# Kernel optimization log

Measured on AMD Instinct MI355X. Metric: run time of the kernel, lower is better.

Reference implementation:

```python
import jax, jax.numpy as jnp
import numpy as np

B, C, H, W = 1, 512, 64, 64
HEADS, DH = 8, 64
DI = HEADS * DH          # 512 = heads * dim_head
SW = 8                   # sliding window size
CB = 16                  # compress block size
SB = 2                   # selection block size
NSEL = 2                 # num selected blocks
N = H * W                # 4096 tokens
NCB = N // CB            # 256 compress blocks
NFB = N // SB            # 2048 fine (selection) blocks
NEG = jnp.finfo(jnp.float32).min


def setup_inputs() -> dict:
    key = jax.random.key(0)
    ks = jax.random.split(key, 24)
    rn = lambda k, shape, s=0.03: jax.random.normal(k, shape, jnp.float32) * s
    return dict(
        x=jax.random.normal(ks[0], (B, C, H, W), jnp.float32),
        w_in=rn(ks[1], (C, C)), b_in=jnp.zeros((C,), jnp.float32),
        g_norm=jnp.ones((C,), jnp.float32),
        wq=rn(ks[2], (DI, C)), wk=rn(ks[3], (DI, C)), wv=rn(ks[4], (DI, C)),
        k_pos=rn(ks[5], (HEADS, CB, DH), 0.02), v_pos=rn(ks[6], (HEADS, CB, DH), 0.02),
        mem_k=rn(ks[7], (HEADS, 1, DH), 0.02), mem_v=rn(ks[8], (HEADS, 1, DH), 0.02),
        kc_w1=rn(ks[9], (CB * DH, CB * DH)), kc_b1=jnp.zeros((CB * DH,), jnp.float32),
        kc_w2=rn(ks[10], (DH, CB * DH)), kc_b2=jnp.zeros((DH,), jnp.float32),
        vc_w1=rn(ks[11], (CB * DH, CB * DH)), vc_b1=jnp.zeros((CB * DH,), jnp.float32),
        vc_w2=rn(ks[12], (DH, CB * DH)), vc_b2=jnp.zeros((DH,), jnp.float32),
        w_strat=rn(ks[13], (3 * HEADS, C)), b_strat=jnp.zeros((3 * HEADS,), jnp.float32),
        w_comb=rn(ks[14], (C, DI)),
        w_out=rn(ks[15], (C, C)), b_out=jnp.zeros((C,), jnp.float32),
    )


def _rope(x):
    # rotary-embedding-torch default: theta=10000, interleaved pairs
    d = x.shape[-1]
    inv = 1.0 / (10000.0 ** (jnp.arange(0, d, 2, dtype=jnp.float32) / d))
    ang = jnp.arange(x.shape[-2], dtype=jnp.float32)[:, None] * inv  # (n, d/2)
    cos = jnp.repeat(jnp.cos(ang), 2, axis=-1)
    sin = jnp.repeat(jnp.sin(ang), 2, axis=-1)
    xp = x.reshape(x.shape[:-1] + (d // 2, 2))
    xr = jnp.stack((-xp[..., 1], xp[..., 0]), axis=-1).reshape(x.shape)
    return x * cos + xr * sin


def reference(x, w_in, b_in, g_norm, wq, wk, wv, k_pos, v_pos, mem_k, mem_v,
              kc_w1, kc_b1, kc_w2, kc_b2, vc_w1, vc_b1, vc_w2, vc_b2,
              w_strat, b_strat, w_comb, w_out, b_out):
    scale = DH ** -0.5
    # proj_in (1x1 conv) then flatten to sequence (b, n, c); residual uses this
    xs = jnp.einsum('bchw,oc->bohw', x, w_in) + b_in[None, :, None, None]
    seq = xs.reshape(B, C, N).transpose(0, 2, 1)
    # RMSNorm
    h = seq * jax.lax.rsqrt(jnp.mean(seq * seq, -1, keepdims=True) + 1e-6) * g_norm
    # qkv -> (b, heads, n, d)
    q = (h @ wq.T).reshape(B, N, HEADS, DH).transpose(0, 2, 1, 3)
    k = (h @ wk.T).reshape(B, N, HEADS, DH).transpose(0, 2, 1, 3)
    v = (h @ wv.T).reshape(B, N, HEADS, DH).transpose(0, 2, 1, 3)

    # ---- 1. compressed attention (block compression MLP + mem kv) ----
    kin = (k + jnp.tile(k_pos, (1, NCB, 1))[None]).reshape(B, HEADS, NCB, CB * DH)
    vin = (v + jnp.tile(v_pos, (1, NCB, 1))[None]).reshape(B, HEADS, NCB, CB * DH)
    ck = jax.nn.relu(kin @ kc_w1.T + kc_b1) @ kc_w2.T + kc_b2   # (b,h,NCB,d)
    cv = jax.nn.relu(vin @ vc_w1.T + vc_b1) @ vc_w2.T + vc_b2
    ck = jnp.concatenate([jnp.broadcast_to(mem_k[None], (B, HEADS, 1, DH)), ck], axis=2)
    cv = jnp.concatenate([jnp.broadcast_to(mem_v[None], (B, HEADS, 1, DH)), cv], axis=2)
    ck_seq = jnp.concatenate([jnp.array([-1]), (jnp.arange(NCB) + 1) * CB - 1])
    cmask = ck_seq[None, :] < jnp.arange(N)[:, None]             # (N, NCB+1), True=attend
    csim = jnp.einsum('bhid,bhjd->bhij', q, ck) * scale
    csim = jnp.where(cmask[None, None], csim, NEG)
    compressed_out = jnp.einsum('bhij,bhjd->bhid', jax.nn.softmax(csim, axis=-1), cv)

    # rotary positions for fine + sliding branches
    rq, rk = _rope(q), _rope(k)

    # ---- 2. fine selection attention ----
    # importance at fine-block granularity; since SB divides CB, each fine block
    # maps to exactly one compress block (equivalent to repeat->mask->mean in torch)
    imp = csim[..., 1:]                                          # drop mem kv logits
    fb_of = jnp.arange(NFB) // (CB // SB)
    imp_fine = imp[..., fb_of]                                   # (b,h,N,NFB)
    blk_causal = jnp.arange(NFB)[None, :] < (jnp.arange(N) // SB)[:, None]
    imp_fine = jnp.where(blk_causal[None, None], imp_fine, -jnp.inf)
    logits = jnp.concatenate([jnp.full((B, HEADS, N, 1), -1e3, jnp.float32), imp_fine], axis=-1)
    probs = jax.nn.softmax(logits, axis=-1)[..., 1:]             # (b,h,N,NFB)
    sel_val, sel_idx = jax.lax.top_k(probs, NSEL)                # (b,h,N,NSEL)
    diag_idx = jnp.broadcast_to((jnp.arange(N) // SB)[None, None, :, None], (B, HEADS, N, 1))
    sel_idx = jnp.concatenate([sel_idx, diag_idx], axis=-1)      # append own (diagonal) block
    fmask_sel = jnp.repeat((sel_val > 1e-10)[..., None], SB, axis=-1)   # (b,h,N,NSEL,SB)
    diag_mask = jnp.arange(SB)[None, :] <= (jnp.arange(N) % SB)[:, None]  # within-block causal
    diag_mask = jnp.broadcast_to(diag_mask[None, None, :, None, :], (B, HEADS, N, 1, SB))
    fmask = jnp.concatenate([fmask_sel, diag_mask], axis=-2).reshape(B, HEADS, N, (NSEL + 1) * SB)
    fk_blk = rk.reshape(B, HEADS, NFB, SB, DH)
    fv_blk = v.reshape(B, HEADS, NFB, SB, DH)
    idx = sel_idx.reshape(B, HEADS, N * (NSEL + 1))[..., None, None]
    fk = jnp.take_along_axis(fk_blk, idx, axis=2).reshape(B, HEADS, N, (NSEL + 1) * SB, DH)
    fv = jnp.take_along_axis(fv_blk, idx, axis=2).reshape(B, HEADS, N, (NSEL + 1) * SB, DH)
    fsim = jnp.einsum('bhid,bhijd->bhij', rq, fk) * scale
    fsim = jnp.where(fmask, fsim, NEG)
    fine_out = jnp.einsum('bhij,bhijd->bhid', jax.nn.softmax(fsim, axis=-1), fv)

    # ---- 3. sliding window attention (causal, exact window: 0 <= i-j <= SW) ----
    kp = jnp.pad(rk, ((0, 0), (0, 0), (SW, 0), (0, 0)))
    vp = jnp.pad(v, ((0, 0), (0, 0), (SW, 0), (0, 0)))
    widx = jnp.arange(N)[:, None] + jnp.arange(SW + 1)[None, :]  # indices into padded seq
    kw = kp[:, :, widx]                                          # (b,h,N,SW+1,d)
    vw = vp[:, :, widx]
    wvalid = (jnp.arange(N)[:, None] - SW + jnp.arange(SW + 1)[None, :]) >= 0
    ssim = jnp.einsum('bhid,bhijd->bhij', rq, kw) * scale
    ssim = jnp.where(wvalid[None, None], ssim, NEG)
    slide_out = jnp.einsum('bhij,bhijd->bhid', jax.nn.softmax(ssim, axis=-1), vw)

    # ---- combine the three strategies with learned sigmoid gates ----
    gates = jax.nn.sigmoid(h @ w_strat.T + b_strat).reshape(B, N, HEADS, 3).transpose(0, 2, 1, 3)
    out = gates[..., 0:1] * compressed_out + gates[..., 1:2] * fine_out + gates[..., 2:3] * slide_out
    out = out.transpose(0, 2, 1, 3).reshape(B, N, DI) @ w_comb.T  # merge heads + combine
    out2d = out.transpose(0, 2, 1).reshape(B, C, H, W)
    return jnp.einsum('bchw,oc->bohw', out2d, w_out) + b_out[None, :, None, None] + xs
```

## Files before the change

kernel.cpp:

```cpp
#include <hip/hip_runtime.h>
#include <hip/hip_bf16.h>
#include <math.h>

typedef __attribute__((ext_vector_type(8))) short s8v;
typedef __attribute__((ext_vector_type(8))) _Float16 h8v;
typedef __attribute__((ext_vector_type(4))) float f4v;
typedef __hip_bfloat16 bf16;

#define NEGF (-3.40282346638528859812e+38f)
#define QSMEM 10240
#define BSMEM 10240

enum { EPI_F32 = 0, EPI_BIAS, EPI_BRELU_BF16, EPI_BF16, EPI_FINAL };

__device__ __forceinline__ float wred_sum(float v) {
#pragma unroll
  for (int m = 1; m < 64; m <<= 1) v += __shfl_xor(v, m, 64);
  return v;
}

template <int EPI>
__device__ __forceinline__ void bgemm_body(char* smem, int bx, int by, int bz,
    const bf16* __restrict__ A, const bf16* __restrict__ B, void* __restrict__ C,
    int K, int ldC, long sA, long sB, long sC,
    const float* __restrict__ bias, const void* __restrict__ aux) {
  short (*Bhs)[2560] = (short(*)[2560])smem;
  const short* ah = (const short*)A + (long)bz * sA;
  const short* bh = (const short*)B + (long)bz * sB;
  int tid = threadIdx.x;
  int wv_ = tid >> 6, lane = tid & 63;
  int lrow = tid >> 2, lcol = (tid & 3) << 3;
  int lidx = lrow * 40 + lcol;
  long bbase = (long)(by * 64 + lrow) * K + lcol;
  int frow = lane & 15, fk = (lane >> 4) << 3;
  long aga = (long)(bx * 64 + wv_ * 16 + frow) * K + fk;
  f4v acc[4] = {};
  { *(s8v*)&Bhs[0][lidx] = *(const s8v*)&bh[bbase]; }
  __syncthreads();
  int nit = K >> 5, buf = 0;
  s8v rA, rB, sE, sO;
  sE = *(const s8v*)&ah[aga];
  if (nit > 1) {
    rA = *(const s8v*)&bh[bbase + 32];
    sO = *(const s8v*)&ah[aga + 32];
  }
#define B_MFMA(sreg)                                                   \
  {                                                                    \
    _Pragma("unroll") for (int nt = 0; nt < 4; nt++) {                 \
      s8v bfh = *(const s8v*)&Bhs[buf][(nt * 16 + frow) * 40 + fk];    \
      acc[nt] = __builtin_amdgcn_mfma_f32_16x16x32_bf16(sreg, bfh, acc[nt], 0, 0, 0); \
    }                                                                  \
  }
  for (int it = 0; it < nit; it += 2) {
    if (it + 2 < nit) rB = *(const s8v*)&bh[bbase + ((long)(it + 2) << 5)];
    B_MFMA(sE)
    if (it + 2 < nit) sE = *(const s8v*)&ah[aga + ((long)(it + 2) << 5)];
    if (it + 1 < nit) {
      *(s8v*)&Bhs[buf ^ 1][lidx] = rA;
      __syncthreads();
      buf ^= 1;
      if (it + 3 < nit) rA = *(const s8v*)&bh[bbase + ((long)(it + 3) << 5)];
      B_MFMA(sO)
      if (it + 3 < nit) sO = *(const s8v*)&ah[aga + ((long)(it + 3) << 5)];
      if (it + 2 < nit) {
        *(s8v*)&Bhs[buf ^ 1][lidx] = rB;
        __syncthreads();
        buf ^= 1;
      }
    }
  }
#undef B_MFMA
  int rb = bx * 64 + wv_ * 16 + ((lane >> 4) << 2);
#pragma unroll
  for (int nt = 0; nt < 4; nt++) {
    int gn = by * 64 + nt * 16 + (lane & 15);
#pragma unroll
    for (int rg = 0; rg < 4; rg++) {
      int gm = rb + rg;
      float v = acc[nt][rg];
      long ci = (long)bz * sC + (long)gm * ldC + gn;
      if (EPI == EPI_F32) ((float*)C)[ci] = v;
      else if (EPI == EPI_BIAS) ((float*)C)[ci] = v + bias[gn];
      else if (EPI == EPI_BRELU_BF16) ((bf16*)C)[ci] = __float2bfloat16(fmaxf(v + bias[gn], 0.f));
      else if (EPI == EPI_BF16) ((bf16*)C)[ci] = __float2bfloat16(v);
      else if (EPI == EPI_FINAL)
        ((float*)C)[ci] = v + bias[gm] + ((const float*)aux)[(long)gn * 512 + gm];
    }
  }
}


#define HX_DECL                                                     \
  short* L = (short*)smem;                                          \
  const int MS = 64 * 40;                                           \
  int tid = threadIdx.x;                                            \
  int wv = tid >> 6, lane = tid & 63;                               \
  int lrow = tid >> 2, lcol = (tid & 3) << 3;                       \
  int frow = lane & 15, fk = (lane >> 4) << 3;                      \
  int soff = lrow * 40 + lcol;                                      \
  f4v acc0[4] = {}, accx[4] = {};

#define HX_STAGE0                                                   \
  {                                                                 \
    *(h8v*)&L[soff] = *(const h8v*)&Bh[bbase];                      \
    *(h8v*)&L[MS + soff] = *(const h8v*)&Bl[bbase];                 \
  }                                                                 \
  __syncthreads();

#define HX_MFMA(sah, sal)                                           \
  {                                                                 \
    _Pragma("unroll") for (int nt = 0; nt < 4; nt++) {              \
      int bo = (nt * 16 + frow) * 40 + fk;                          \
      h8v bh_ = *(const h8v*)&L[bo];                                \
      h8v bl_ = *(const h8v*)&L[MS + bo];                           \
      acc0[nt] = __builtin_amdgcn_mfma_f32_16x16x32_f16(sah, bh_, acc0[nt], 0, 0, 0); \
      accx[nt] = __builtin_amdgcn_mfma_f32_16x16x32_f16(sah, bl_, accx[nt], 0, 0, 0); \
      accx[nt] = __builtin_amdgcn_mfma_f32_16x16x32_f16(sal, bh_, accx[nt], 0, 0, 0); \
    }                                                               \
  }

#define HX_LOOP(NIT)                                                \
  h8v rAh, rAl, rBh, rBl, sEh, sEl, sOh, sOl;                       \
  sEh = *(const h8v*)&Ah[aga];                                      \
  sEl = *(const h8v*)&Al[aga];                                      \
  if ((NIT) > 1) {                                                  \
    rAh = *(const h8v*)&Bh[bbase + 32];                             \
    rAl = *(const h8v*)&Bl[bbase + 32];                             \
    sOh = *(const h8v*)&Ah[aga + 32];                               \
    sOl = *(const h8v*)&Al[aga + 32];                               \
  }                                                                 \
  for (int it = 0; it < (NIT); it += 2) {                           \
    if (it + 2 < (NIT)) {                                           \
      long ko = (long)(it + 2) << 5;                                \
      rBh = *(const h8v*)&Bh[bbase + ko];                           \
      rBl = *(const h8v*)&Bl[bbase + ko];                           \
    }                                                               \
    HX_MFMA(sEh, sEl)                                               \
    if (it + 2 < (NIT)) {                                           \
      long ko = (long)(it + 2) << 5;                                \
      sEh = *(const h8v*)&Ah[aga + ko];                             \
      sEl = *(const h8v*)&Al[aga + ko];                             \
    }                                                               \
    if (it + 1 < (NIT)) {                                           \
      __syncthreads();                                              \
      *(h8v*)&L[soff] = rAh;                                        \
      *(h8v*)&L[MS + soff] = rAl;                                   \
      __syncthreads();                                              \
      if (it + 3 < (NIT)) {                                         \
        long ko = (long)(it + 3) << 5;                              \
        rAh = *(const h8v*)&Bh[bbase + ko];                         \
        rAl = *(const h8v*)&Bl[bbase + ko];                         \
      }                                                             \
      HX_MFMA(sOh, sOl)                                             \
      if (it + 3 < (NIT)) {                                         \
        long ko = (long)(it + 3) << 5;                              \
        sOh = *(const h8v*)&Ah[aga + ko];                           \
        sOl = *(const h8v*)&Al[aga + ko];                           \
      }                                                             \
      if (it + 2 < (NIT)) {                                         \
        __syncthreads();                                            \
        *(h8v*)&L[soff] = rBh;                                      \
        *(h8v*)&L[MS + soff] = rBl;                                 \
        __syncthreads();                                            \
      }                                                             \
    }                                                               \
  }

#define HX_COMBINE(nt, rg) (acc0[nt][rg] + accx[nt][rg] * (1.f / 4096.f))

__device__ __forceinline__ void qk_f16_body(char* smem, int bx, int by,
    const _Float16* __restrict__ Ah, const _Float16* __restrict__ Al,
    const _Float16* __restrict__ Bh, const _Float16* __restrict__ Bl,
    _Float16* __restrict__ qhh, _Float16* __restrict__ qhl,
    _Float16* __restrict__ kinh, _Float16* __restrict__ kinl,
    float* __restrict__ rq, float* __restrict__ rk, const float* __restrict__ kpos,
    const float2* __restrict__ ropet) {
  HX_DECL
  long aga = (long)(bx * 64 + wv * 16 + frow) * 512 + fk;
  long bbase = (long)(by * 64 + lrow) * 512 + lcol;
  HX_STAGE0
  HX_LOOP(16)
  bool isq = by < 8;
  int h = by & 7;
  int rb = wv * 16 + ((lane >> 4) << 2);
#pragma unroll
  for (int nt = 0; nt < 4; nt++) {
    int dloc = nt * 16 + frow;
    int d2 = dloc >> 1;
#pragma unroll
    for (int rg = 0; rg < 4; rg++) {
      int n = bx * 64 + rb + rg;
      float vf = HX_COMBINE(nt, rg);
      float2 cs = ropet[(long)n * 32 + d2];
      float sv = cs.x, cv = cs.y;
      float vp = __shfl_xor(vf, 1, 64);
      float rr = (dloc & 1) ? (vf * cv + vp * sv) : (vf * cv - vp * sv);
      long oi = ((long)h * 4096 + n) * 64 + dloc;
      if (isq) {
        _Float16 hi = (_Float16)vf;
        qhh[oi] = hi;
        qhl[oi] = (_Float16)((vf - (float)hi) * 4096.f);
        rq[oi] = rr;
      } else {
        rk[oi] = rr;
        float kv = vf + kpos[(h * 16 + (n & 15)) * 64 + dloc];
        _Float16 khi = (_Float16)kv;
        long ki = (((long)h * 256 + (n >> 4)) * 16 + (n & 15)) * 64 + dloc;
        kinh[ki] = khi;
        kinl[ki] = (_Float16)((kv - (float)khi) * 4096.f);
      }
    }
  }
}

__device__ __forceinline__ void hx_conv_body(char* smem, int bx, int by,
    const _Float16* __restrict__ Ah, const _Float16* __restrict__ Al,
    const _Float16* __restrict__ Bh, const _Float16* __restrict__ Bl,
    float* __restrict__ C, const float* __restrict__ bias) {
  HX_DECL
  long aga = (long)(bx * 64 + wv * 16 + frow) * 512 + fk;
  long bbase = (long)(by * 64 + lrow) * 512 + lcol;
  HX_STAGE0
  HX_LOOP(16)
  int rb = bx * 64 + wv * 16 + ((lane >> 4) << 2);
#pragma unroll
  for (int nt = 0; nt < 4; nt++) {
    int gn = by * 64 + nt * 16 + frow;
#pragma unroll
    for (int rg = 0; rg < 4; rg++) {
      int gm = rb + rg;
      C[(long)gm * 512 + gn] = HX_COMBINE(nt, rg) + bias[gn];
    }
  }
}

__device__ __forceinline__ void hx_mlp1_body(char* smem, int bx, int by,
    const _Float16* __restrict__ Ah, const _Float16* __restrict__ Al,
    const _Float16* __restrict__ Bh, const _Float16* __restrict__ Bl,
    _Float16* __restrict__ Ch, _Float16* __restrict__ Cl, const float* __restrict__ bias) {
  HX_DECL
  long aga = (long)(bx * 64 + wv * 16 + frow) * 1024 + fk;
  long bbase = (long)(by * 64 + lrow) * 1024 + lcol;
  HX_STAGE0
  HX_LOOP(32)
  int rb = bx * 64 + wv * 16 + ((lane >> 4) << 2);
#pragma unroll
  for (int nt = 0; nt < 4; nt++) {
    int gn = by * 64 + nt * 16 + frow;
#pragma unroll
    for (int rg = 0; rg < 4; rg++) {
      int gm = rb + rg;
      float v = fmaxf(HX_COMBINE(nt, rg) + bias[gn], 0.f);
      _Float16 hi = (_Float16)v;
      long ci = (long)gm * 1024 + gn;
      Ch[ci] = hi;
      Cl[ci] = (_Float16)((v - (float)hi) * 4096.f);
    }
  }
}

__device__ __forceinline__ void hx_ksplit_body(char* smem, int bx, int by,
    const _Float16* __restrict__ Ah, const _Float16* __restrict__ Al,
    const _Float16* __restrict__ Bh, const _Float16* __restrict__ Bl,
    float* __restrict__ P) {
  HX_DECL
  long kbeg = (long)by << 7;
  long aga = (long)(bx * 64 + wv * 16 + frow) * 1024 + kbeg + fk;
  long bbase = (long)lrow * 1024 + kbeg + lcol;
  HX_STAGE0
  HX_LOOP(4)
  float* p = P + (long)by * 131072;
  int rb = bx * 64 + wv * 16 + ((lane >> 4) << 2);
#pragma unroll
  for (int nt = 0; nt < 4; nt++) {
    int gn = nt * 16 + frow;
#pragma unroll
    for (int rg = 0; rg < 4; rg++) {
      int gm = rb + rg;
      p[(long)gm * 64 + gn] = HX_COMBINE(nt, rg);
    }
  }
}

__device__ __forceinline__ void hx_csim_body(char* smem, int bx, int by, int bz,
    const _Float16* __restrict__ Ah, const _Float16* __restrict__ Al,
    const _Float16* __restrict__ Bh, const _Float16* __restrict__ Bl,
    float* __restrict__ C) {
  HX_DECL
  long aga = ((long)bz * 4096 + bx * 64 + wv * 16 + frow) * 64 + fk;
  long bbase = ((long)bz * 320 + by * 64 + lrow) * 64 + lcol;
  HX_STAGE0
  HX_LOOP(2)
  int rb = bx * 64 + wv * 16 + ((lane >> 4) << 2);
#pragma unroll
  for (int nt = 0; nt < 4; nt++) {
    int gn = by * 64 + nt * 16 + frow;
#pragma unroll
    for (int rg = 0; rg < 4; rg++) {
      int gm = rb + rg;
      C[((long)bz * 4096 + gm) * 320 + gn] = HX_COMBINE(nt, rg) * 0.125f;
    }
  }
}

__device__ __forceinline__ void prep_elem(long i,
    const float* __restrict__ wq, const float* __restrict__ wk, const float* __restrict__ wv,
    const float* __restrict__ wst, const float* __restrict__ bst,
    const float* __restrict__ kc_w1, const float* __restrict__ kc_w2,
    const float* __restrict__ vc_w1, const float* __restrict__ vc_w2, const float* __restrict__ w_comb,
    const float* __restrict__ w_out, _Float16* __restrict__ wqkh, _Float16* __restrict__ wqkl,
    bf16* __restrict__ wvs, float* __restrict__ bias2,
    _Float16* __restrict__ kw1h, _Float16* __restrict__ kw1l,
    _Float16* __restrict__ kw2h, _Float16* __restrict__ kw2l, bf16* __restrict__ vw1b,
    bf16* __restrict__ vw2b, bf16* __restrict__ wcombb, bf16* __restrict__ woutb) {
  if (i < 524288) {
    int r = (int)(i >> 9), c = (int)(i & 511);
    float w = (r < 512) ? wq[i] : wk[(r - 512) * 512 + c];
    _Float16 hi = (_Float16)w;
    wqkh[i] = hi;
    wqkl[i] = (_Float16)((w - (float)hi) * 4096.f);
    return;
  }
  i -= 524288;
  if (i < 294912) {
    int r = (int)(i >> 9), c = (int)(i & 511);
    float v = 0.f;
    if (r < 512) v = wv[i];
    else if (r < 536) v = wst[(r - 512) * 512 + c];
    wvs[i] = __float2bfloat16(v);
    if (i < 576) bias2[i] = (i >= 512 && i < 536) ? bst[i - 512] : 0.f;
    return;
  }
  i -= 294912;
  if (i < 1048576) {
    float w = kc_w1[i];
    _Float16 hi = (_Float16)w;
    kw1h[i] = hi;
    kw1l[i] = (_Float16)((w - (float)hi) * 4096.f);
    return;
  }
  i -= 1048576;
  if (i < 65536) {
    float w = kc_w2[i];
    _Float16 hi = (_Float16)w;
    kw2h[i] = hi;
    kw2l[i] = (_Float16)((w - (float)hi) * 4096.f);
    return;
  }
  i -= 65536;
  if (i < 1048576) { vw1b[i] = __float2bfloat16(vc_w1[i]); return; }
  i -= 1048576;
  if (i < 65536) { vw2b[i] = __float2bfloat16(vc_w2[i]); return; }
  i -= 65536;
  if (i < 262144) { wcombb[i] = __float2bfloat16(w_comb[i]); return; }
  i -= 262144;
  if (i < 262144) woutb[i] = __float2bfloat16(w_out[i]);
}
#define PREP_TOTAL 3571712l

template <int EPI>
__global__ __launch_bounds__(256) void gemm_bt(
    const bf16* __restrict__ A, const bf16* __restrict__ B, void* __restrict__ C,
    int K, int ldC, long sA, long sB, long sC,
    const float* __restrict__ bias, const void* __restrict__ aux) {
  __shared__ char smem[BSMEM];
  bgemm_body<EPI>(smem, blockIdx.x, blockIdx.y, blockIdx.z, A, B, C, K, ldC, sA, sB, sC, bias, aux);
}

__global__ __launch_bounds__(256) void k_conv_prep(
    const _Float16* __restrict__ xth, const _Float16* __restrict__ xtl,
    const _Float16* __restrict__ winh, const _Float16* __restrict__ winl,
    float* __restrict__ xsf, const float* __restrict__ b_in,
    const float* __restrict__ wq, const float* __restrict__ wk, const float* __restrict__ wv,
    const float* __restrict__ wst, const float* __restrict__ bst,
    const float* __restrict__ kc_w1, const float* __restrict__ kc_w2,
    const float* __restrict__ vc_w1, const float* __restrict__ vc_w2, const float* __restrict__ w_comb,
    const float* __restrict__ w_out, _Float16* __restrict__ wqkh, _Float16* __restrict__ wqkl,
    bf16* __restrict__ wvs, float* __restrict__ bias2,
    _Float16* __restrict__ kw1h, _Float16* __restrict__ kw1l,
    _Float16* __restrict__ kw2h, _Float16* __restrict__ kw2l, bf16* __restrict__ vw1b,
    bf16* __restrict__ vw2b, bf16* __restrict__ wcombb, bf16* __restrict__ woutb) {
  __shared__ char smem[QSMEM];
  if (blockIdx.y < 8) {
    hx_conv_body(smem, blockIdx.x, blockIdx.y, xth, xtl, winh, winl, xsf, b_in);
  } else {
    long base = (((long)(blockIdx.y - 8) * 64 + blockIdx.x) * 256) + threadIdx.x;
    for (long i = base; i < PREP_TOTAL; i += 16l * 64 * 256)
      prep_elem(i, wq, wk, wv, wst, bst, kc_w1, kc_w2, vc_w1, vc_w2, w_comb, w_out,
                wqkh, wqkl, wvs, bias2, kw1h, kw1l, kw2h, kw2l, vw1b, vw2b, wcombb, woutb);
  }
}

__global__ __launch_bounds__(256) void k_fused_qk_t2(
    const _Float16* __restrict__ hhi, const _Float16* __restrict__ hlo,
    const _Float16* __restrict__ wqkh, const _Float16* __restrict__ wqkl,
    _Float16* __restrict__ qhh, _Float16* __restrict__ qhl,
    _Float16* __restrict__ kinh, _Float16* __restrict__ kinl,
    float* __restrict__ rq, float* __restrict__ rk, const float* __restrict__ kpos,
    const float2* __restrict__ ropet,
    const bf16* __restrict__ hbf, const bf16* __restrict__ wvs, float* __restrict__ T2,
    const float* __restrict__ bias2) {
  __shared__ char smem[QSMEM];
  if (blockIdx.y >= 16) {
    bgemm_body<EPI_BIAS>(smem, blockIdx.x, blockIdx.y - 16, 0, hbf, wvs, T2, 512, 576, 0, 0, 0, bias2,
                         nullptr);
    return;
  }
  qk_f16_body(smem, blockIdx.x, blockIdx.y, hhi, hlo, wqkh, wqkl, qhh, qhl, kinh, kinl, rq, rk, kpos,
              ropet);
}

__global__ void k_repackV(const float* __restrict__ T2, const float* __restrict__ vpos,
                          float* __restrict__ vvv, bf16* __restrict__ vin) {
  int e = blockIdx.x * 256 + threadIdx.x;
  int d = e & 63, n = (e >> 6) & 4095, h = e >> 18;
  float v0 = T2[(long)n * 576 + h * 64 + d];
  vvv[((long)h * 4096 + n) * 64 + d] = v0;
  vin[(((long)h * 256 + (n >> 4)) * 16 + (n & 15)) * 64 + d] =
      __float2bfloat16(v0 + vpos[(h * 16 + (n & 15)) * 64 + d]);
}

__global__ __launch_bounds__(256) void k_fused_mlp1(
    const _Float16* __restrict__ kinh, const _Float16* __restrict__ kinl,
    const _Float16* __restrict__ kw1h, const _Float16* __restrict__ kw1l,
    _Float16* __restrict__ hidh, _Float16* __restrict__ hidl, const float* __restrict__ kb1,
    const bf16* __restrict__ vin, const bf16* __restrict__ vw1,
    bf16* __restrict__ hidv, const float* __restrict__ vb1) {
  __shared__ char smem[QSMEM];
  if (blockIdx.y < 16)
    hx_mlp1_body(smem, blockIdx.x, blockIdx.y, kinh, kinl, kw1h, kw1l, hidh, hidl, kb1);
  else
    bgemm_body<EPI_BRELU_BF16>(smem, blockIdx.x, blockIdx.y - 16, 0, vin, vw1, hidv, 1024, 1024, 0, 0, 0,
                               vb1, nullptr);
}

__global__ __launch_bounds__(256) void k_fused_mlp2(
    const _Float16* __restrict__ hidh, const _Float16* __restrict__ hidl,
    const _Float16* __restrict__ kw2h, const _Float16* __restrict__ kw2l, float* __restrict__ kpart,
    const bf16* __restrict__ hidv, const bf16* __restrict__ vw2, float* __restrict__ cvc,
    const float* __restrict__ vb2) {
  __shared__ char smem[QSMEM];
  if (blockIdx.y < 8)
    hx_ksplit_body(smem, blockIdx.x, blockIdx.y, hidh, hidl, kw2h, kw2l, kpart);
  else
    bgemm_body<EPI_BIAS>(smem, blockIdx.x, 0, 0, hidv, vw2, cvc, 1024, 64, 0, 0, 0, vb2, nullptr);
}

__global__ __launch_bounds__(256) void k_csim(
    const _Float16* __restrict__ qhh, const _Float16* __restrict__ qhl,
    const _Float16* __restrict__ ckbh, const _Float16* __restrict__ ckbl, float* __restrict__ csim) {
  if (blockIdx.y * 64 > blockIdx.x * 4 + 3) return;
  __shared__ char smem[QSMEM];
  hx_csim_body(smem, blockIdx.x, blockIdx.y, blockIdx.z, qhh, qhl, ckbh, ckbl, csim);
}

__global__ void k_transpose16(const float* __restrict__ x, _Float16* __restrict__ xth,
                              _Float16* __restrict__ xtl,
                              const float* __restrict__ w_in, _Float16* __restrict__ winh,
                              _Float16* __restrict__ winl, float2* __restrict__ ropet) {
  if (blockIdx.y == 16) {
    int tid = threadIdx.y * 32 + threadIdx.x;
    long base = (long)blockIdx.x * 256 + tid;
    for (long i = base; i < 393216; i += 128l * 256) {
      if (i < 262144) {
        float w = w_in[i];
        _Float16 hi = (_Float16)w;
        winh[i] = hi;
        winl[i] = (_Float16)((w - (float)hi) * 4096.f);
      } else {
        int idx = (int)(i - 262144);
        int d2 = idx & 31, n = idx >> 5;
        float inv = exp2f((float)d2 * -0.4152410118609203f);
        float sv, cv;
        sincosf((float)n * inv, &sv, &cv);
        ropet[idx] = make_float2(sv, cv);
      }
    }
    return;
  }
  __shared__ float t[32][33];
  int n0 = blockIdx.x * 32, c0 = blockIdx.y * 32;
  int tx = threadIdx.x, ty = threadIdx.y;
#pragma unroll
  for (int r = ty; r < 32; r += 8) t[r][tx] = x[(long)(c0 + r) * 4096 + n0 + tx];
  __syncthreads();
#pragma unroll
  for (int r = ty; r < 32; r += 8) {
    float v = t[tx][r];
    _Float16 hi = (_Float16)v;
    long o = (long)(n0 + r) * 512 + c0 + tx;
    xth[o] = hi;
    xtl[o] = (_Float16)((v - (float)hi) * 4096.f);
  }
}

__global__ __launch_bounds__(256) void k_rmsnorm(const float* __restrict__ xs, const float* __restrict__ g,
                                                 _Float16* __restrict__ hhi, _Float16* __restrict__ hlo,
                                                 bf16* __restrict__ hbf) {
  int n = blockIdx.x, t = threadIdx.x;
  const float* row = xs + (long)n * 512;
  double a = (double)row[t], b = (double)row[t + 256];
  double ss = a * a + b * b;
#pragma unroll
  for (int m = 1; m < 64; m <<= 1) ss += __shfl_xor(ss, m, 64);
  __shared__ double red[4];
  if ((t & 63) == 0) red[t >> 6] = ss;
  __syncthreads();
  double tot = red[0] + red[1] + red[2] + red[3];
  double r = 1.0 / sqrt(tot / 512.0 + 1e-6);
  double h0 = a * r * (double)g[t], h1 = b * r * (double)g[t + 256];
  long o = (long)n * 512 + t;
  float f0 = (float)h0, f1 = (float)h1;
  _Float16 a0 = (_Float16)f0, a1 = (_Float16)f1;
  hhi[o] = a0;
  hhi[o + 256] = a1;
  hlo[o] = (_Float16)((f0 - (float)a0) * 4096.f);
  hlo[o + 256] = (_Float16)((f1 - (float)a1) * 4096.f);
  hbf[o] = __float2bfloat16(f0);
  hbf[o + 256] = __float2bfloat16(f1);
}

__global__ void k_repackB(const float* __restrict__ kpart, const float* __restrict__ cvc,
                          const float* __restrict__ mem_k, const float* __restrict__ mem_v,
                          const float* __restrict__ kb2, _Float16* __restrict__ ckbh,
                          _Float16* __restrict__ ckbl, bf16* __restrict__ cvtb) {
  int g = blockIdx.x * 256 + threadIdx.x;
  if (g < 8 * 320 * 64) {
    int d = g & 63, j = (g >> 6) % 320, h = g / (320 * 64);
    float vf = 0.f;
    if (j == 0) vf = mem_k[h * 64 + d];
    else if (j < 257) {
      long ri = ((long)h * 256 + (j - 1)) * 64 + d;
      double s = 0.0;
#pragma unroll
      for (int p = 0; p < 8; p++) s += (double)kpart[(long)p * 131072 + ri];
      vf = (float)(s + (double)kb2[d]);
    }
    _Float16 hi = (_Float16)vf;
    ckbh[g] = hi;
    ckbl[g] = (_Float16)((vf - (float)hi) * 4096.f);
  }
  if (g < 8 * 64 * 288) {
    int j = g % 288, d = (g / 288) & 63, h = g / (288 * 64);
    float v = 0.f;
    if (j == 0) v = mem_v[h * 64 + d];
    else if (j < 257) v = cvc[((long)h * 256 + (j - 1)) * 64 + d];
    cvtb[g] = __float2bfloat16(v);
  }
}

__global__ __launch_bounds__(256) void k_selsm(const float* __restrict__ csim, bf16* __restrict__ pb,
                                               int4* __restrict__ selb) {
  int r = blockIdx.x * 4 + (threadIdx.x >> 6);
  int lane = threadIdx.x & 63;
  int i = r & 4095;
  const float* row = csim + (long)r * 320;
  int nv = i / 16 + 1;
  float s[5], e[5];
  float mx = -INFINITY;
#pragma unroll
  for (int t = 0; t < 5; t++) {
    int j = lane + 64 * t;
    float v = (j < nv) ? row[j] : -INFINITY;
    s[t] = v;
    mx = fmaxf(mx, v);
  }
#pragma unroll
  for (int m = 1; m < 64; m <<= 1) mx = fmaxf(mx, __shfl_xor(mx, m, 64));
  float sum = 0.f;
#pragma unroll
  for (int t = 0; t < 5; t++) {
    int j = lane + 64 * t;
    e[t] = (j < nv) ? __expf(s[t] - mx) : 0.f;
    sum += e[t];
  }
  sum = wred_sum(sum);
  float rinv = 1.f / sum;
  bf16* prow = pb + (long)r * 288;
#pragma unroll
  for (int t = 0; t < 5; t++) {
    int j = lane + 64 * t;
    if (j < 288) prow[j] = __float2bfloat16((j < nv) ? e[t] * rinv : 0.f);
  }
  int nvb = i >> 1;
  int nmv = (nvb + 7) >> 3;
  float vm[4];
  float bestv = -INFINITY;
  int bestm = 0x7fffffff;
#pragma unroll
  for (int t = 0; t < 4; t++) {
    int m = lane + 64 * t;
    float v = -INFINITY;
    if (m < nmv) v = (m + 1 < nv) ? row[m + 1] : NEGF;
    vm[t] = v;
    if (v > bestv) { bestv = v; bestm = m; }
  }
#pragma unroll
  for (int mk = 1; mk < 64; mk <<= 1) {
    float ov = __shfl_xor(bestv, mk, 64);
    int om = __shfl_xor(bestm, mk, 64);
    if (ov > bestv || (ov == bestv && om < bestm)) { bestv = ov; bestm = om; }
  }
  int m0 = bestm;
  int cnt0 = min(8, nvb - 8 * m0);
  float rv = -INFINITY;
  int rm = 0x7fffffff;
#pragma unroll
  for (int t = 0; t < 4; t++) {
    int m = lane + 64 * t;
    if (m != m0 && vm[t] > rv) { rv = vm[t]; rm = m; }
  }
#pragma unroll
  for (int mk = 1; mk < 64; mk <<= 1) {
    float ov = __shfl_xor(rv, mk, 64);
    int om = __shfl_xor(rm, mk, 64);
    if (ov > rv || (ov == rv && om < rm)) { rv = ov; rm = om; }
  }
  float Ml = fmaxf(-1000.f, bestv);
  float z = 0.f;
#pragma unroll
  for (int t = 0; t < 4; t++) {
    int m = lane + 64 * t;
    if (m < nmv) z += (float)min(8, nvb - 8 * m) * expf(vm[t] - Ml);
  }
  z = wred_sum(z) + expf(-1000.f - Ml);
  int fb0 = 0, fb1 = 0, mk0 = 0, mk1 = 0;
  if (nmv > 0) {
    float sv0 = expf(bestv - Ml) / z;
    fb0 = 8 * m0;
    mk0 = sv0 > 1e-10f;
    if (cnt0 >= 2) { fb1 = fb0 + 1; mk1 = mk0; }
    else if (nmv > 1) {
      float sv1 = expf(rv - Ml) / z;
      fb1 = 8 * rm;
      mk1 = sv1 > 1e-10f;
    }
  }
  if (lane == 0) selb[r] = make_int4(fb0, fb1, mk0, mk1);
}

__global__ __launch_bounds__(256) void k_fineslide(const float* __restrict__ rq, const float* __restrict__ rk,
                                                   const float* __restrict__ vv, const float* __restrict__ co,
                                                   const int4* __restrict__ selb, const float* __restrict__ T2,
                                                   bf16* __restrict__ comb) {
  int r = blockIdx.x * 4 + (threadIdx.x >> 6);
  int d = threadIdx.x & 63;
  int h = r >> 12, i = r & 4095;
  long hb = (long)h * 4096 * 64;
  float qd = rq[hb + (long)i * 64 + d];
  int4 s4 = selb[r];
  int dg = i >> 1;
  int tok[6] = {2 * s4.x, 2 * s4.x + 1, 2 * s4.y, 2 * s4.y + 1, 2 * dg, 2 * dg + 1};
  int ok6[6] = {s4.z, s4.z, s4.w, s4.w, 1, (i & 1)};
  float sim[6], val[6];
#pragma unroll
  for (int j = 0; j < 6; j++) {
    float kd = rk[hb + (long)tok[j] * 64 + d];
    val[j] = vv[hb + (long)tok[j] * 64 + d];
    float p = wred_sum(qd * kd);
    sim[j] = ok6[j] ? p * 0.125f : NEGF;
  }
  float mx = sim[0];
#pragma unroll
  for (int j = 1; j < 6; j++) mx = fmaxf(mx, sim[j]);
  float den = 0.f, fo = 0.f;
#pragma unroll
  for (int j = 0; j < 6; j++) {
    float e_ = __expf(sim[j] - mx);
    den += e_;
    fo += e_ * val[j];
  }
  fo /= den;
  float ssim[9], sval[9];
#pragma unroll
  for (int t = 0; t < 9; t++) {
    int tk = i - 8 + t;
    int okt = tk >= 0;
    int tc = okt ? tk : 0;
    float kd = rk[hb + (long)tc * 64 + d];
    sval[t] = okt ? vv[hb + (long)tc * 64 + d] : 0.f;
    float p = wred_sum(qd * kd);
    ssim[t] = okt ? p * 0.125f : NEGF;
  }
  float mx2 = ssim[8];
#pragma unroll
  for (int t = 0; t < 8; t++) mx2 = fmaxf(mx2, ssim[t]);
  float den2 = 0.f, so = 0.f;
#pragma unroll
  for (int t = 0; t < 9; t++) {
    float e_ = __expf(ssim[t] - mx2);
    den2 += e_;
    so += e_ * sval[t];
  }
  so /= den2;
  const float* gb = T2 + (long)i * 576 + 512 + h * 3;
  float g0 = 1.f / (1.f + __expf(-gb[0]));
  float g1 = 1.f / (1.f + __expf(-gb[1]));
  float g2 = 1.f / (1.f + __expf(-gb[2]));
  float cd = co[hb + (long)i * 64 + d];
  comb[(long)i * 512 + h * 64 + d] = __float2bfloat16(g0 * cd + g1 * fo + g2 * so);
}

extern "C" void kernel_launch(void* const* d_in, const int* in_sizes, int n_in, void* d_out, int out_size,
                              void* d_ws, size_t ws_size, hipStream_t stream) {
  (void)in_sizes; (void)n_in; (void)out_size; (void)ws_size;
  const float* x = (const float*)d_in[0];
  const float* w_in = (const float*)d_in[1];
  const float* b_in = (const float*)d_in[2];
  const float* g_norm = (const float*)d_in[3];
  const float* wq = (const float*)d_in[4];
  const float* wk = (const float*)d_in[5];
  const float* wv = (const float*)d_in[6];
  const float* k_pos = (const float*)d_in[7];
  const float* v_pos = (const float*)d_in[8];
  const float* mem_k = (const float*)d_in[9];
  const float* mem_v = (const float*)d_in[10];
  const float* kc_w1 = (const float*)d_in[11];
  const float* kc_b1 = (const float*)d_in[12];
  const float* kc_w2 = (const float*)d_in[13];
  const float* kc_b2 = (const float*)d_in[14];
  const float* vc_w1 = (const float*)d_in[15];
  const float* vc_b1 = (const float*)d_in[16];
  const float* vc_w2 = (const float*)d_in[17];
  const float* vc_b2 = (const float*)d_in[18];
  const float* w_strat = (const float*)d_in[19];
  const float* b_strat = (const float*)d_in[20];
  const float* w_comb = (const float*)d_in[21];
  const float* w_out = (const float*)d_in[22];
  const float* b_out = (const float*)d_in[23];

  char* wsp = (char*)d_ws;
  size_t off = 0;
  auto alloc = [&](size_t b) -> void* {
    void* p = wsp + off;
    off += (b + 255) & ~(size_t)255;
    return p;
  };
  float* xsf = (float*)alloc(4096l * 512 * 4);
  _Float16* hhi = (_Float16*)alloc(4096l * 512 * 2);
  _Float16* hlo = (_Float16*)alloc(4096l * 512 * 2);
  bf16* hbf = (bf16*)alloc(4096l * 512 * 2);
  _Float16* winh = (_Float16*)alloc(512l * 512 * 2);
  _Float16* winl = (_Float16*)alloc(512l * 512 * 2);
  _Float16* wqkh = (_Float16*)alloc(1024l * 512 * 2);
  _Float16* wqkl = (_Float16*)alloc(1024l * 512 * 2);
  bf16* wvs = (bf16*)alloc(576l * 512 * 2);
  float* bias2 = (float*)alloc(576 * 4);
  float2* ropet = (float2*)alloc(4096l * 32 * 8);
  float* T2 = (float*)alloc(4096l * 576 * 4);
  float* csim = (float*)alloc(8l * 4096 * 320 * 4);
  _Float16* qhh = (_Float16*)alloc(8l * 4096 * 64 * 2);
  _Float16* qhl = (_Float16*)alloc(8l * 4096 * 64 * 2);
  float* rq = (float*)alloc(8l * 4096 * 64 * 4);
  float* rk = (float*)alloc(8l * 4096 * 64 * 4);
  float* vvb = (float*)alloc(8l * 4096 * 64 * 4);
  char* xthl = (char*)alloc(2l * 4096 * 512 * 2);
  _Float16* xth = (_Float16*)xthl;
  _Float16* xtl = xth + 4096l * 512;
  _Float16* hidh = xth;
  _Float16* hidl = xtl;
  char* kinpb = (char*)alloc(2048l * 1024 * 8 + 2048l * 1024 * 2);
  _Float16* kinh = (_Float16*)kinpb;
  _Float16* kinl = kinh + 2048l * 1024;
  bf16* vinb = (bf16*)(kinpb + 2l * 2048 * 1024 * 2);
  bf16* pb = (bf16*)kinpb;
  _Float16* kw1h = (_Float16*)alloc(1024l * 1024 * 2);
  _Float16* kw1l = (_Float16*)alloc(1024l * 1024 * 2);
  _Float16* kw2h = (_Float16*)alloc(64l * 1024 * 2);
  _Float16* kw2l = (_Float16*)alloc(64l * 1024 * 2);
  bf16* vw1b = (bf16*)alloc(1024l * 1024 * 2);
  bf16* vw2b = (bf16*)alloc(64l * 1024 * 2);
  bf16* hidv = (bf16*)alloc(2048l * 1024 * 2);
  float* cvc = (float*)alloc(2048l * 64 * 4);
  _Float16* ckbh = (_Float16*)alloc(8l * 320 * 64 * 2);
  _Float16* ckbl = (_Float16*)alloc(8l * 320 * 64 * 2);
  bf16* cvtb = (bf16*)alloc(8l * 64 * 288 * 2);
  int4* selb = (int4*)alloc(32768l * 16);
  float* co = (float*)alloc(8l * 4096 * 64 * 4);
  bf16* comb = (bf16*)alloc(4096l * 512 * 2);
  bf16* zb = (bf16*)alloc(4096l * 512 * 2);
  bf16* wcombb = (bf16*)alloc(512l * 512 * 2);
  bf16* woutb = (bf16*)alloc(512l * 512 * 2);
  float* kpart = (float*)alloc(8l * 2048 * 64 * 4);

  k_transpose16<<<dim3(128, 17), dim3(32, 8), 0, stream>>>(x, xth, xtl, w_in, winh, winl, ropet);
  k_conv_prep<<<dim3(64, 24), 256, 0, stream>>>(xth, xtl, winh, winl, xsf, b_in, wq, wk, wv, w_strat,
                                                b_strat, kc_w1, kc_w2, vc_w1, vc_w2, w_comb, w_out,
                                                wqkh, wqkl, wvs, bias2, kw1h, kw1l, kw2h, kw2l,
                                                vw1b, vw2b, wcombb, woutb);
  k_rmsnorm<<<4096, 256, 0, stream>>>(xsf, g_norm, hhi, hlo, hbf);
  k_fused_qk_t2<<<dim3(64, 25, 1), 256, 0, stream>>>(hhi, hlo, wqkh, wqkl, qhh, qhl, kinh, kinl, rq, rk,
                                                     k_pos, ropet, hbf, wvs, T2, bias2);
  k_repackV<<<8192, 256, 0, stream>>>(T2, v_pos, vvb, vinb);
  k_fused_mlp1<<<dim3(32, 32, 1), 256, 0, stream>>>(kinh, kinl, kw1h, kw1l, hidh, hidl, kc_b1, vinb, vw1b,
                                                    hidv, vc_b1);
  k_fused_mlp2<<<dim3(32, 9, 1), 256, 0, stream>>>(hidh, hidl, kw2h, kw2l, kpart, hidv, vw2b, cvc, vc_b2);
  k_repackB<<<640, 256, 0, stream>>>(kpart, cvc, mem_k, mem_v, kc_b2, ckbh, ckbl, cvtb);
  k_csim<<<dim3(64, 5, 8), 256, 0, stream>>>(qhh, qhl, ckbh, ckbl, csim);
  k_selsm<<<8192, 256, 0, stream>>>(csim, pb, selb);
  gemm_bt<EPI_F32><<<dim3(64, 1, 8), 256, 0, stream>>>(pb, cvtb, co, 288, 64, 4096l * 288, 64l * 288,
                                                       4096l * 64, nullptr, nullptr);
  k_fineslide<<<8192, 256, 0, stream>>>(rq, rk, vvb, co, selb, T2, comb);
  gemm_bt<EPI_BF16><<<dim3(64, 8, 1), 256, 0, stream>>>(comb, wcombb, zb, 512, 512, 0, 0, 0, nullptr, nullptr);
  gemm_bt<EPI_FINAL><<<dim3(8, 64, 1), 256, 0, stream>>>(woutb, zb, d_out, 512, 4096, 0, 0, 0, b_out, xsf);
}
```

Measured before the change: 332.7 us.

## Double M-tile per block in split-f16 MFMA GEMMs to reuse staged B tiles

Each block of the hi/lo f16 MFMA GEMMs (conv, qk, mlp1, ksplit, csim) now computes 128 rows of A instead of 64. Every B tile staged in shared memory is therefore used by two sets of accumulators. Grids are not resized in most launchers; surplus blocks return early, and the csim launch grid is halved with its causal skip condition adjusted. This cuts B-tile loads and barriers per output but doubles accumulator registers, which may lower occupancy and leaves fewer active blocks for the GPU's many CUs.

```diff
diff --git a/kernel.cpp b/kernel.cpp
--- a/kernel.cpp
+++ b/kernel.cpp
@@ -90,7 +90,7 @@
 }
 
 
-#define HX_DECL                                                     \
+#define HX2_DECL                                                    \
   short* L = (short*)smem;                                          \
   const int MS = 64 * 40;                                           \
   int tid = threadIdx.x;                                            \
@@ -98,7 +98,7 @@
   int lrow = tid >> 2, lcol = (tid & 3) << 3;                       \
   int frow = lane & 15, fk = (lane >> 4) << 3;                      \
   int soff = lrow * 40 + lcol;                                      \
-  f4v acc0[4] = {}, accx[4] = {};
+  f4v acc0[2][4] = {}, accx[2][4] = {};
 
 #define HX_STAGE0                                                   \
   {                                                                 \
@@ -107,27 +107,35 @@
   }                                                                 \
   __syncthreads();
 
-#define HX_MFMA(sah, sal)                                           \
+#define HX2_MFMA(h0, l0, h1, l1)                                    \
   {                                                                 \
     _Pragma("unroll") for (int nt = 0; nt < 4; nt++) {              \
       int bo = (nt * 16 + frow) * 40 + fk;                          \
       h8v bh_ = *(const h8v*)&L[bo];                                \
       h8v bl_ = *(const h8v*)&L[MS + bo];                           \
-      acc0[nt] = __builtin_amdgcn_mfma_f32_16x16x32_f16(sah, bh_, acc0[nt], 0, 0, 0); \
-      accx[nt] = __builtin_amdgcn_mfma_f32_16x16x32_f16(sah, bl_, accx[nt], 0, 0, 0); \
-      accx[nt] = __builtin_amdgcn_mfma_f32_16x16x32_f16(sal, bh_, accx[nt], 0, 0, 0); \
+      acc0[0][nt] = __builtin_amdgcn_mfma_f32_16x16x32_f16(h0, bh_, acc0[0][nt], 0, 0, 0); \
+      accx[0][nt] = __builtin_amdgcn_mfma_f32_16x16x32_f16(h0, bl_, accx[0][nt], 0, 0, 0); \
+      accx[0][nt] = __builtin_amdgcn_mfma_f32_16x16x32_f16(l0, bh_, accx[0][nt], 0, 0, 0); \
+      acc0[1][nt] = __builtin_amdgcn_mfma_f32_16x16x32_f16(h1, bh_, acc0[1][nt], 0, 0, 0); \
+      accx[1][nt] = __builtin_amdgcn_mfma_f32_16x16x32_f16(h1, bl_, accx[1][nt], 0, 0, 0); \
+      accx[1][nt] = __builtin_amdgcn_mfma_f32_16x16x32_f16(l1, bh_, accx[1][nt], 0, 0, 0); \
     }                                                               \
   }
 
-#define HX_LOOP(NIT)                                                \
-  h8v rAh, rAl, rBh, rBl, sEh, sEl, sOh, sOl;                       \
-  sEh = *(const h8v*)&Ah[aga];                                      \
-  sEl = *(const h8v*)&Al[aga];                                      \
+#define HX2_LOOP(NIT)                                               \
+  h8v rAh, rAl, rBh, rBl;                                           \
+  h8v sEh0, sEl0, sEh1, sEl1, sOh0, sOl0, sOh1, sOl1;               \
+  sEh0 = *(const h8v*)&Ah[aga];                                     \
+  sEl0 = *(const h8v*)&Al[aga];                                     \
+  sEh1 = *(const h8v*)&Ah[ag2];                                     \
+  sEl1 = *(const h8v*)&Al[ag2];                                     \
   if ((NIT) > 1) {                                                  \
     rAh = *(const h8v*)&Bh[bbase + 32];                             \
     rAl = *(const h8v*)&Bl[bbase + 32];                             \
-    sOh = *(const h8v*)&Ah[aga + 32];                               \
-    sOl = *(const h8v*)&Al[aga + 32];                               \
+    sOh0 = *(const h8v*)&Ah[aga + 32];                              \
+    sOl0 = *(const h8v*)&Al[aga + 32];                              \
+    sOh1 = *(const h8v*)&Ah[ag2 + 32];                              \
+    sOl1 = *(const h8v*)&Al[ag2 + 32];                              \
   }                                                                 \
   for (int it = 0; it < (NIT); it += 2) {                           \
     if (it + 2 < (NIT)) {                                           \
@@ -135,11 +143,13 @@
       rBh = *(const h8v*)&Bh[bbase + ko];                           \
       rBl = *(const h8v*)&Bl[bbase + ko];                           \
     }                                                               \
-    HX_MFMA(sEh, sEl)                                               \
+    HX2_MFMA(sEh0, sEl0, sEh1, sEl1)                                \
     if (it + 2 < (NIT)) {                                           \
       long ko = (long)(it + 2) << 5;                                \
-      sEh = *(const h8v*)&Ah[aga + ko];                             \
-      sEl = *(const h8v*)&Al[aga + ko];                             \
+      sEh0 = *(const h8v*)&Ah[aga + ko];                            \
+      sEl0 = *(const h8v*)&Al[aga + ko];                            \
+      sEh1 = *(const h8v*)&Ah[ag2 + ko];                            \
+      sEl1 = *(const h8v*)&Al[ag2 + ko];                            \
     }                                                               \
     if (it + 1 < (NIT)) {                                           \
       __syncthreads();                                              \
@@ -151,11 +161,13 @@
         rAh = *(const h8v*)&Bh[bbase + ko];                         \
         rAl = *(const h8v*)&Bl[bbase + ko];                         \
       }                                                             \
-      HX_MFMA(sOh, sOl)                                             \
+      HX2_MFMA(sOh0, sOl0, sOh1, sOl1)                              \
       if (it + 3 < (NIT)) {                                         \
         long ko = (long)(it + 3) << 5;                              \
-        sOh = *(const h8v*)&Ah[aga + ko];                           \
-        sOl = *(const h8v*)&Al[aga + ko];                           \
+        sOh0 = *(const h8v*)&Ah[aga + ko];                          \
+        sOl0 = *(const h8v*)&Al[aga + ko];                          \
+        sOh1 = *(const h8v*)&Ah[ag2 + ko];                          \
+        sOl1 = *(const h8v*)&Al[ag2 + ko];                          \
       }                                                             \
       if (it + 2 < (NIT)) {                                         \
         __syncthreads();                                            \
@@ -166,7 +178,7 @@
     }                                                               \
   }
 
-#define HX_COMBINE(nt, rg) (acc0[nt][rg] + accx[nt][rg] * (1.f / 4096.f))
+#define HX2_COMBINE(g, nt, rg) (acc0[g][nt][rg] + accx[g][nt][rg] * (1.f / 4096.f))
 
 __device__ __forceinline__ void qk_f16_body(char* smem, int bx, int by,
     const _Float16* __restrict__ Ah, const _Float16* __restrict__ Al,
@@ -175,39 +187,43 @@
     _Float16* __restrict__ kinh, _Float16* __restrict__ kinl,
     float* __restrict__ rq, float* __restrict__ rk, const float* __restrict__ kpos,
     const float2* __restrict__ ropet) {
-  HX_DECL
-  long aga = (long)(bx * 64 + wv * 16 + frow) * 512 + fk;
+  HX2_DECL
+  long aga = (long)(bx * 128 + wv * 16 + frow) * 512 + fk;
+  long ag2 = aga + 64l * 512;
   long bbase = (long)(by * 64 + lrow) * 512 + lcol;
   HX_STAGE0
-  HX_LOOP(16)
+  HX2_LOOP(16)
   bool isq = by < 8;
   int h = by & 7;
   int rb = wv * 16 + ((lane >> 4) << 2);
 #pragma unroll
-  for (int nt = 0; nt < 4; nt++) {
-    int dloc = nt * 16 + frow;
-    int d2 = dloc >> 1;
-#pragma unroll
-    for (int rg = 0; rg < 4; rg++) {
-      int n = bx * 64 + rb + rg;
-      float vf = HX_COMBINE(nt, rg);
-      float2 cs = ropet[(long)n * 32 + d2];
-      float sv = cs.x, cv = cs.y;
-      float vp = __shfl_xor(vf, 1, 64);
-      float rr = (dloc & 1) ? (vf * cv + vp * sv) : (vf * cv - vp * sv);
-      long oi = ((long)h * 4096 + n) * 64 + dloc;
-      if (isq) {
-        _Float16 hi = (_Float16)vf;
-        qhh[oi] = hi;
-        qhl[oi] = (_Float16)((vf - (float)hi) * 4096.f);
-        rq[oi] = rr;
-      } else {
-        rk[oi] = rr;
-        float kv = vf + kpos[(h * 16 + (n & 15)) * 64 + dloc];
-        _Float16 khi = (_Float16)kv;
-        long ki = (((long)h * 256 + (n >> 4)) * 16 + (n & 15)) * 64 + dloc;
-        kinh[ki] = khi;
-        kinl[ki] = (_Float16)((kv - (float)khi) * 4096.f);
+  for (int g = 0; g < 2; g++) {
+#pragma unroll
+    for (int nt = 0; nt < 4; nt++) {
+      int dloc = nt * 16 + frow;
+      int d2 = dloc >> 1;
+#pragma unroll
+      for (int rg = 0; rg < 4; rg++) {
+        int n = bx * 128 + g * 64 + rb + rg;
+        float vf = HX2_COMBINE(g, nt, rg);
+        float2 cs = ropet[(long)n * 32 + d2];
+        float sv = cs.x, cv = cs.y;
+        float vp = __shfl_xor(vf, 1, 64);
+        float rr = (dloc & 1) ? (vf * cv + vp * sv) : (vf * cv - vp * sv);
+        long oi = ((long)h * 4096 + n) * 64 + dloc;
+        if (isq) {
+          _Float16 hi = (_Float16)vf;
+          qhh[oi] = hi;
+          qhl[oi] = (_Float16)((vf - (float)hi) * 4096.f);
+          rq[oi] = rr;
+        } else {
+          rk[oi] = rr;
+          float kv = vf + kpos[(h * 16 + (n & 15)) * 64 + dloc];
+          _Float16 khi = (_Float16)kv;
+          long ki = (((long)h * 256 + (n >> 4)) * 16 + (n & 15)) * 64 + dloc;
+          kinh[ki] = khi;
+          kinl[ki] = (_Float16)((kv - (float)khi) * 4096.f);
+        }
       }
     }
   }
@@ -217,19 +233,23 @@
     const _Float16* __restrict__ Ah, const _Float16* __restrict__ Al,
     const _Float16* __restrict__ Bh, const _Float16* __restrict__ Bl,
     float* __restrict__ C, const float* __restrict__ bias) {
-  HX_DECL
-  long aga = (long)(bx * 64 + wv * 16 + frow) * 512 + fk;
+  HX2_DECL
+  long aga = (long)(bx * 128 + wv * 16 + frow) * 512 + fk;
+  long ag2 = aga + 64l * 512;
   long bbase = (long)(by * 64 + lrow) * 512 + lcol;
   HX_STAGE0
-  HX_LOOP(16)
-  int rb = bx * 64 + wv * 16 + ((lane >> 4) << 2);
-#pragma unroll
-  for (int nt = 0; nt < 4; nt++) {
-    int gn = by * 64 + nt * 16 + frow;
-#pragma unroll
-    for (int rg = 0; rg < 4; rg++) {
-      int gm = rb + rg;
-      C[(long)gm * 512 + gn] = HX_COMBINE(nt, rg) + bias[gn];
+  HX2_LOOP(16)
+  int rb = bx * 128 + wv * 16 + ((lane >> 4) << 2);
+#pragma unroll
+  for (int g = 0; g < 2; g++) {
+#pragma unroll
+    for (int nt = 0; nt < 4; nt++) {
+      int gn = by * 64 + nt * 16 + frow;
+#pragma unroll
+      for (int rg = 0; rg < 4; rg++) {
+        int gm = rb + g * 64 + rg;
+        C[(long)gm * 512 + gn] = HX2_COMBINE(g, nt, rg) + bias[gn];
+      }
     }
   }
 }
@@ -238,23 +258,27 @@
     const _Float16* __restrict__ Ah, const _Float16* __restrict__ Al,
     const _Float16* __restrict__ Bh, const _Float16* __restrict__ Bl,
     _Float16* __restrict__ Ch, _Float16* __restrict__ Cl, const float* __restrict__ bias) {
-  HX_DECL
-  long aga = (long)(bx * 64 + wv * 16 + frow) * 1024 + fk;
+  HX2_DECL
+  long aga = (long)(bx * 128 + wv * 16 + frow) * 1024 + fk;
+  long ag2 = aga + 64l * 1024;
   long bbase = (long)(by * 64 + lrow) * 1024 + lcol;
   HX_STAGE0
-  HX_LOOP(32)
-  int rb = bx * 64 + wv * 16 + ((lane >> 4) << 2);
-#pragma unroll
-  for (int nt = 0; nt < 4; nt++) {
-    int gn = by * 64 + nt * 16 + frow;
-#pragma unroll
-    for (int rg = 0; rg < 4; rg++) {
-      int gm = rb + rg;
-      float v = fmaxf(HX_COMBINE(nt, rg) + bias[gn], 0.f);
-      _Float16 hi = (_Float16)v;
-      long ci = (long)gm * 1024 + gn;
-      Ch[ci] = hi;
-      Cl[ci] = (_Float16)((v - (float)hi) * 4096.f);
+  HX2_LOOP(32)
+  int rb = bx * 128 + wv * 16 + ((lane >> 4) << 2);
+#pragma unroll
+  for (int g = 0; g < 2; g++) {
+#pragma unroll
+    for (int nt = 0; nt < 4; nt++) {
+      int gn = by * 64 + nt * 16 + frow;
+#pragma unroll
+      for (int rg = 0; rg < 4; rg++) {
+        int gm = rb + g * 64 + rg;
+        float v = fmaxf(HX2_COMBINE(g, nt, rg) + bias[gn], 0.f);
+        _Float16 hi = (_Float16)v;
+        long ci = (long)gm * 1024 + gn;
+        Ch[ci] = hi;
+        Cl[ci] = (_Float16)((v - (float)hi) * 4096.f);
+      }
     }
   }
 }
@@ -263,21 +287,25 @@
     const _Float16* __restrict__ Ah, const _Float16* __restrict__ Al,
     const _Float16* __restrict__ Bh, const _Float16* __restrict__ Bl,
     float* __restrict__ P) {
-  HX_DECL
+  HX2_DECL
   long kbeg = (long)by << 7;
-  long aga = (long)(bx * 64 + wv * 16 + frow) * 1024 + kbeg + fk;
+  long aga = (long)(bx * 128 + wv * 16 + frow) * 1024 + kbeg + fk;
+  long ag2 = aga + 64l * 1024;
   long bbase = (long)lrow * 1024 + kbeg + lcol;
   HX_STAGE0
-  HX_LOOP(4)
+  HX2_LOOP(4)
   float* p = P + (long)by * 131072;
-  int rb = bx * 64 + wv * 16 + ((lane >> 4) << 2);
-#pragma unroll
-  for (int nt = 0; nt < 4; nt++) {
-    int gn = nt * 16 + frow;
-#pragma unroll
-    for (int rg = 0; rg < 4; rg++) {
-      int gm = rb + rg;
-      p[(long)gm * 64 + gn] = HX_COMBINE(nt, rg);
+  int rb = bx * 128 + wv * 16 + ((lane >> 4) << 2);
+#pragma unroll
+  for (int g = 0; g < 2; g++) {
+#pragma unroll
+    for (int nt = 0; nt < 4; nt++) {
+      int gn = nt * 16 + frow;
+#pragma unroll
+      for (int rg = 0; rg < 4; rg++) {
+        int gm = rb + g * 64 + rg;
+        p[(long)gm * 64 + gn] = HX2_COMBINE(g, nt, rg);
+      }
     }
   }
 }
@@ -286,19 +314,23 @@
     const _Float16* __restrict__ Ah, const _Float16* __restrict__ Al,
     const _Float16* __restrict__ Bh, const _Float16* __restrict__ Bl,
     float* __restrict__ C) {
-  HX_DECL
-  long aga = ((long)bz * 4096 + bx * 64 + wv * 16 + frow) * 64 + fk;
+  HX2_DECL
+  long aga = ((long)bz * 4096 + bx * 128 + wv * 16 + frow) * 64 + fk;
+  long ag2 = aga + 64l * 64;
   long bbase = ((long)bz * 320 + by * 64 + lrow) * 64 + lcol;
   HX_STAGE0
-  HX_LOOP(2)
-  int rb = bx * 64 + wv * 16 + ((lane >> 4) << 2);
-#pragma unroll
-  for (int nt = 0; nt < 4; nt++) {
-    int gn = by * 64 + nt * 16 + frow;
-#pragma unroll
-    for (int rg = 0; rg < 4; rg++) {
-      int gm = rb + rg;
-      C[((long)bz * 4096 + gm) * 320 + gn] = HX_COMBINE(nt, rg) * 0.125f;
+  HX2_LOOP(2)
+  int rb = bx * 128 + wv * 16 + ((lane >> 4) << 2);
+#pragma unroll
+  for (int g = 0; g < 2; g++) {
+#pragma unroll
+    for (int nt = 0; nt < 4; nt++) {
+      int gn = by * 64 + nt * 16 + frow;
+#pragma unroll
+      for (int rg = 0; rg < 4; rg++) {
+        int gm = rb + g * 64 + rg;
+        C[((long)bz * 4096 + gm) * 320 + gn] = HX2_COMBINE(g, nt, rg) * 0.125f;
+      }
     }
   }
 }
@@ -382,6 +414,7 @@
     bf16* __restrict__ vw2b, bf16* __restrict__ wcombb, bf16* __restrict__ woutb) {
   __shared__ char smem[QSMEM];
   if (blockIdx.y < 8) {
+    if (blockIdx.x >= 32) return;
     hx_conv_body(smem, blockIdx.x, blockIdx.y, xth, xtl, winh, winl, xsf, b_in);
   } else {
     long base = (((long)(blockIdx.y - 8) * 64 + blockIdx.x) * 256) + threadIdx.x;
@@ -406,6 +439,7 @@
                          nullptr);
     return;
   }
+  if (blockIdx.x >= 32) return;
   qk_f16_body(smem, blockIdx.x, blockIdx.y, hhi, hlo, wqkh, wqkl, qhh, qhl, kinh, kinl, rq, rk, kpos,
               ropet);
 }
@@ -427,11 +461,13 @@
     const bf16* __restrict__ vin, const bf16* __restrict__ vw1,
     bf16* __restrict__ hidv, const float* __restrict__ vb1) {
   __shared__ char smem[QSMEM];
-  if (blockIdx.y < 16)
+  if (blockIdx.y < 16) {
+    if (blockIdx.x >= 16) return;
     hx_mlp1_body(smem, blockIdx.x, blockIdx.y, kinh, kinl, kw1h, kw1l, hidh, hidl, kb1);
-  else
+  } else {
     bgemm_body<EPI_BRELU_BF16>(smem, blockIdx.x, blockIdx.y - 16, 0, vin, vw1, hidv, 1024, 1024, 0, 0, 0,
                                vb1, nullptr);
+  }
 }
 
 __global__ __launch_bounds__(256) void k_fused_mlp2(
@@ -440,16 +476,18 @@
     const bf16* __restrict__ hidv, const bf16* __restrict__ vw2, float* __restrict__ cvc,
     const float* __restrict__ vb2) {
   __shared__ char smem[QSMEM];
-  if (blockIdx.y < 8)
+  if (blockIdx.y < 8) {
+    if (blockIdx.x >= 16) return;
     hx_ksplit_body(smem, blockIdx.x, blockIdx.y, hidh, hidl, kw2h, kw2l, kpart);
-  else
+  } else {
     bgemm_body<EPI_BIAS>(smem, blockIdx.x, 0, 0, hidv, vw2, cvc, 1024, 64, 0, 0, 0, vb2, nullptr);
+  }
 }
 
 __global__ __launch_bounds__(256) void k_csim(
     const _Float16* __restrict__ qhh, const _Float16* __restrict__ qhl,
     const _Float16* __restrict__ ckbh, const _Float16* __restrict__ ckbl, float* __restrict__ csim) {
-  if (blockIdx.y * 64 > blockIdx.x * 4 + 3) return;
+  if (blockIdx.y * 64 > blockIdx.x * 8 + 7) return;
   __shared__ char smem[QSMEM];
   hx_csim_body(smem, blockIdx.x, blockIdx.y, blockIdx.z, qhh, qhl, ckbh, ckbl, csim);
 }
@@ -796,7 +834,7 @@
                                                     hidv, vc_b1);
   k_fused_mlp2<<<dim3(32, 9, 1), 256, 0, stream>>>(hidh, hidl, kw2h, kw2l, kpart, hidv, vw2b, cvc, vc_b2);
   k_repackB<<<640, 256, 0, stream>>>(kpart, cvc, mem_k, mem_v, kc_b2, ckbh, ckbl, cvtb);
-  k_csim<<<dim3(64, 5, 8), 256, 0, stream>>>(qhh, qhl, ckbh, ckbl, csim);
+  k_csim<<<dim3(32, 5, 8), 256, 0, stream>>>(qhh, qhl, ckbh, ckbl, csim);
   k_selsm<<<8192, 256, 0, stream>>>(csim, pb, selb);
   gemm_bt<EPI_F32><<<dim3(64, 1, 8), 256, 0, stream>>>(pb, cvtb, co, 288, 64, 4096l * 288, 64l * 288,
                                                        4096l * 64, nullptr, nullptr);
```

Result: slower. 363.1 us (+9.1%).
